# Optimization experiments

Hardware: AMD Instinct MI355X
Metric: run time of the kernel (lower is better)

## Reference

```python
import jax, jax.numpy as jnp
import numpy as np

B, S, H, L, NH, F, V, K, R = 64, 512, 256, 4, 8, 1024, 50265, 8, 25
DH = H // NH
EPS = 1e-5


def layernorm(x, g, b):
    mu = x.mean(-1, keepdims=True)
    var = ((x - mu) ** 2).mean(-1, keepdims=True)
    return (x - mu) * jax.lax.rsqrt(var + EPS) * g + b


def setup_inputs() -> dict:
    key = jax.random.key(0)
    ks = jax.random.split(key, 24)
    input_ids = jax.random.randint(ks[0], (B, S), 0, V, dtype=jnp.int64)
    # prefix attention mask with variable valid lengths (ragged sequences)
    lengths = jax.random.randint(ks[1], (B,), 16, S + 1)
    attention_mask = (jnp.arange(S)[None, :] < lengths[:, None]).astype(jnp.int32)
    sub_indices = jax.random.randint(ks[2], (B, K), 0, S, dtype=jnp.int64)
    obj_indices = jax.random.randint(ks[3], (B, K), 0, S, dtype=jnp.int64)
    sub_counts = jax.random.randint(ks[4], (B,), 0, K + 1, dtype=jnp.int32)
    obj_counts = jax.random.randint(ks[5], (B,), 0, K + 1, dtype=jnp.int32)
    sc = 0.02
    p = {
        'emb': jax.random.normal(ks[6], (V, H), jnp.float32) * sc,
        'Wqkv': jax.random.normal(ks[7], (L, H, 3 * H), jnp.float32) * sc,
        'bqkv': jnp.zeros((L, 3 * H), jnp.float32),
        'Wo': jax.random.normal(ks[8], (L, H, H), jnp.float32) * sc,
        'bo': jnp.zeros((L, H), jnp.float32),
        'ln1_g': jnp.ones((L, H), jnp.float32), 'ln1_b': jnp.zeros((L, H), jnp.float32),
        'ln2_g': jnp.ones((L, H), jnp.float32), 'ln2_b': jnp.zeros((L, H), jnp.float32),
        'W1': jax.random.normal(ks[9], (L, H, F), jnp.float32) * sc,
        'b1': jnp.zeros((L, F), jnp.float32),
        'W2': jax.random.normal(ks[10], (L, F, H), jnp.float32) * sc,
        'b2': jnp.zeros((L, H), jnp.float32),
        'lnf_g': jnp.ones((H,), jnp.float32), 'lnf_b': jnp.zeros((H,), jnp.float32),
        'mW1': jax.random.normal(ks[11], (3 * H, H), jnp.float32) * sc,
        'mb1': jnp.zeros((H,), jnp.float32),
        'mW2': jax.random.normal(ks[12], (H, R), jnp.float32) * sc,
        'mb2': jnp.zeros((R,), jnp.float32),
    }
    return dict(input_ids=input_ids, attention_mask=attention_mask,
                sub_indices=sub_indices, sub_counts=sub_counts,
                obj_indices=obj_indices, obj_counts=obj_counts, **p)


def _encoder(input_ids, attention_mask, emb, Wqkv, bqkv, Wo, bo,
             ln1_g, ln1_b, ln2_g, ln2_b, W1, b1, W2, b2, lnf_g, lnf_b):
    x = emb[input_ids]  # [B,S,H]
    kbias = jnp.where(attention_mask[:, None, None, :] > 0, 0.0, -1e9)  # mask keys
    scale = 1.0 / np.sqrt(DH)
    for l in range(L):  # small fixed layer loop
        qkv = x @ Wqkv[l] + bqkv[l]
        q, k, v = jnp.split(qkv, 3, axis=-1)
        q = q.reshape(B, S, NH, DH).transpose(0, 2, 1, 3)
        k = k.reshape(B, S, NH, DH).transpose(0, 2, 1, 3)
        v = v.reshape(B, S, NH, DH).transpose(0, 2, 1, 3)
        scores = jnp.einsum('bhqd,bhkd->bhqk', q, k) * scale + kbias
        attn = jax.nn.softmax(scores, axis=-1)
        o = jnp.einsum('bhqk,bhkd->bhqd', attn, v).transpose(0, 2, 1, 3).reshape(B, S, H)
        x = layernorm(x + o @ Wo[l] + bo[l], ln1_g[l], ln1_b[l])
        h = jax.nn.relu(x @ W1[l] + b1[l]) @ W2[l] + b2[l]
        x = layernorm(x + h, ln2_g[l], ln2_b[l])
    return layernorm(x, lnf_g, lnf_b)


def _pooled(seq, idx, counts):
    g = jnp.take_along_axis(seq, idx[:, :, None], axis=1)  # [B,K,H]
    m = (jnp.arange(K)[None, :] < counts[:, None]).astype(seq.dtype)
    s = (g * m[:, :, None]).sum(1)
    c = counts.astype(seq.dtype)[:, None]
    return jnp.where(c > 0, s / jnp.maximum(c, 1.0), 0.0)  # zeros if no indices


def reference(input_ids, attention_mask, sub_indices, sub_counts, obj_indices, obj_counts,
              emb, Wqkv, bqkv, Wo, bo, ln1_g, ln1_b, ln2_g, ln2_b,
              W1, b1, W2, b2, lnf_g, lnf_b, mW1, mb1, mW2, mb2):
    seq = _encoder(input_ids, attention_mask, emb, Wqkv, bqkv, Wo, bo,
                   ln1_g, ln1_b, ln2_g, ln2_b, W1, b1, W2, b2, lnf_g, lnf_b)
    sub = _pooled(seq, sub_indices, sub_counts)
    obj = _pooled(seq, obj_indices, obj_counts)
    mask = attention_mask.astype(seq.dtype)
    lens = mask.sum(1)[:, None]
    story = jnp.where(lens > 0, (seq * mask[:, :, None]).sum(1) / jnp.maximum(lens, 1.0),
                      seq.mean(1))
    feat = jnp.concatenate([sub, obj, story], axis=-1)  # [B,3H]
    logits = jax.nn.relu(feat @ mW1 + mb1) @ mW2 + mb2
    return logits
```

## Files before the change

kernel.cpp:

```cpp
#include <hip/hip_runtime.h>
#include <hip/hip_bf16.h>


typedef __hip_bfloat16 bf16;
typedef __attribute__((ext_vector_type(8))) short short8;
typedef __attribute__((ext_vector_type(4))) float f32x4;

#define S_LEN 512
#define H_DIM 256
#define NTOK  32768

__device__ __forceinline__ void gload_lds16(const void* g, void* l) {
  __builtin_amdgcn_global_load_lds(
      (const __attribute__((address_space(1))) unsigned int*)g,
      (__attribute__((address_space(3))) unsigned int*)l, 16, 0, 0);
}

__device__ __forceinline__ unsigned short f2bu(float x) {
  bf16 t = __float2bfloat16(x);
  return *reinterpret_cast<unsigned short*>(&t);
}

__global__ __launch_bounds__(64) void lens_kernel(
    const int* __restrict__ amask, int* __restrict__ ntiles,
    int* __restrict__ lenb) {
  const int b = blockIdx.x, t = threadIdx.x;
  int c = 0;
#pragma unroll
  for (int i = 0; i < 8; ++i) c += amask[b * S_LEN + t + i * 64];
#pragma unroll
  for (int off = 1; off < 64; off <<= 1) c += __shfl_xor(c, off);
  if (t == 0) {
    lenb[b] = c;
    ntiles[b] = (c + 63) >> 6;
  }
}

__global__ __launch_bounds__(256) void tcast_kernel(
    const float* __restrict__ in, bf16* __restrict__ out, int K, int N) {
  const int l = blockIdx.z;
  in  += (size_t)l * K * N;
  out += (size_t)l * K * N;
  __shared__ float t[32][33];
  const int n0 = blockIdx.x * 32, k0 = blockIdx.y * 32;
  const int c = threadIdx.x & 31, r = threadIdx.x >> 5;
#pragma unroll
  for (int rr = r; rr < 32; rr += 8)
    t[rr][c] = in[(size_t)(k0 + rr) * N + n0 + c];
  __syncthreads();
#pragma unroll
  for (int rr = r; rr < 32; rr += 8)
    out[(size_t)(n0 + rr) * K + k0 + c] = __float2bfloat16(t[c][rr]);
}

__global__ __launch_bounds__(256) void embed_kernel(
    const int* __restrict__ ids, const float* __restrict__ emb,
    float* __restrict__ X, bf16* __restrict__ Xb) {
  size_t i4 = (size_t)blockIdx.x * 256 + threadIdx.x;
  int tok = (int)(i4 >> 6);
  int d4  = (int)(i4 & 63);
  float4 v = *(const float4*)&emb[(size_t)ids[tok] * H_DIM + d4 * 4];
  *(float4*)&X[i4 * 4] = v;
  ushort4 pk;
  pk.x = f2bu(v.x); pk.y = f2bu(v.y); pk.z = f2bu(v.z); pk.w = f2bu(v.w);
  *(ushort4*)&Xb[i4 * 4] = pk;
}

template<int MODE, bool RELU>
__global__ __launch_bounds__(256) void hgemm_kernel(
    const bf16* __restrict__ A, const bf16* __restrict__ Bt,
    const float* __restrict__ bias, float* __restrict__ Cf,
    bf16* __restrict__ Cb, bf16* __restrict__ Vt,
    int M, int N, int K) {
  __shared__ __align__(16) bf16 As[2][4096];
  __shared__ __align__(16) bf16 Bs[2][4096];
  const int tid = threadIdx.x;
  const int wv = tid >> 6, ln = tid & 63;
  const int fr = ln & 15, g4 = ln >> 4;
  const int wr = wv >> 1, wc = wv & 1;
  const int m0 = blockIdx.y * 128, n0 = blockIdx.x * 128;
  const int lr = tid >> 2, lk = (tid & 3) * 8;

#define STAGE_G(buf, kk) do {                                                  \
    const int kof_ = (kk) * 32;                                                \
    gload_lds16(A  + (size_t)(m0 + lr) * K + kof_ + lk,                        \
                &As[(buf)][wv * 512]);                                         \
    gload_lds16(A  + (size_t)(m0 + 64 + lr) * K + kof_ + lk,                   \
                &As[(buf)][2048 + wv * 512]);                                  \
    gload_lds16(Bt + (size_t)(n0 + lr) * K + kof_ + lk,                        \
                &Bs[(buf)][wv * 512]);                                         \
    gload_lds16(Bt + (size_t)(n0 + 64 + lr) * K + kof_ + lk,                   \
                &Bs[(buf)][2048 + wv * 512]);                                  \
  } while (0)

  f32x4 acc[4][4];
#pragma unroll
  for (int i = 0; i < 4; ++i)
#pragma unroll
    for (int j = 0; j < 4; ++j)
      acc[i][j] = (f32x4){0.f, 0.f, 0.f, 0.f};

  const int NT = K >> 5;
  STAGE_G(0, 0);
  __syncthreads();
  int cur = 0;
  for (int kt = 0; kt < NT; ++kt) {
    if (kt + 1 < NT) STAGE_G(cur ^ 1, kt + 1);
    short8 af[4], bfv[4];
#pragma unroll
    for (int i = 0; i < 4; ++i)
      af[i] = *(const short8*)&As[cur][(wr * 64 + i * 16 + fr) * 32 + g4 * 8];
#pragma unroll
    for (int j = 0; j < 4; ++j)
      bfv[j] = *(const short8*)&Bs[cur][(wc * 64 + j * 16 + fr) * 32 + g4 * 8];
#pragma unroll
    for (int i = 0; i < 4; ++i)
#pragma unroll
      for (int j = 0; j < 4; ++j)
        acc[i][j] = __builtin_amdgcn_mfma_f32_16x16x32_bf16(
            af[i], bfv[j], acc[i][j], 0, 0, 0);
    __syncthreads();
    cur ^= 1;
  }
#undef STAGE_G

  const int crow = g4 * 4, ccol = fr;
#pragma unroll
  for (int j = 0; j < 4; ++j) {
    const int n = n0 + wc * 64 + j * 16 + ccol;
    const float bv = bias[n];
#pragma unroll
    for (int i = 0; i < 4; ++i) {
      const int mbase = m0 + wr * 64 + i * 16 + crow;
#pragma unroll
      for (int r = 0; r < 4; ++r) {
        float o = acc[i][j][r] + bv;
        if (RELU) o = fmaxf(o, 0.f);
        const int m = mbase + r;
        if (MODE == 1) {
          Cb[(size_t)m * N + n] = __float2bfloat16(o);
        } else {
          if (n < 512) {
            Cb[(size_t)m * 768 + n] = __float2bfloat16(o);
          } else {
            const int hd = n - 512, hh = hd >> 5, dd = hd & 31;
            const int bb = m >> 9, ss = m & 511;
            const int ssw = (ss & ~63) | ((ss & 63) ^ ((dd & 7) << 3));
            Vt[(((size_t)bb * 8 + hh) * 32 + dd) * 512 + ssw] =
                __float2bfloat16(o);
          }
        }
      }
    }
  }
}

__global__ __launch_bounds__(256) void hgemm_ln_kernel(
    const bf16* __restrict__ A, const bf16* __restrict__ Bt,
    const float* __restrict__ bias, float* __restrict__ X,
    bf16* __restrict__ Xb, const float* __restrict__ g,
    const float* __restrict__ bt, int K) {
  __shared__ __align__(16) bf16 As[2][2048];
  __shared__ __align__(16) bf16 Bs[2][8192];
  __shared__ float rsum[4][64];
  __shared__ float rsq[4][64];
  const int tid = threadIdx.x;
  const int wv = tid >> 6;
  const int ln = tid & 63;
  const int fr = ln & 15, g4 = ln >> 4;
  const int m0 = blockIdx.x * 64;

#define STAGE_L(buf, kk) do {                                                  \
    const int kof_ = (kk) * 32;                                                \
    gload_lds16(A + (size_t)(m0 + (tid >> 2)) * K + kof_ + (tid & 3) * 8,      \
                &As[(buf)][wv * 512]);                                         \
    _Pragma("unroll")                                                          \
    for (int e = 0; e < 4; ++e) {                                              \
      const int vt = e * 256 + tid;                                            \
      gload_lds16(Bt + (size_t)(vt >> 2) * K + kof_ + (vt & 3) * 8,            \
                  &Bs[(buf)][e * 2048 + wv * 512]);                            \
    }                                                                          \
  } while (0)

  f32x4 acc[4][4];
#pragma unroll
  for (int i = 0; i < 4; ++i)
#pragma unroll
    for (int j = 0; j < 4; ++j)
      acc[i][j] = (f32x4){0.f, 0.f, 0.f, 0.f};

  const int NT = K >> 5;
  STAGE_L(0, 0);
  __syncthreads();
  int cur = 0;
  for (int kt = 0; kt < NT; ++kt) {
    if (kt + 1 < NT) STAGE_L(cur ^ 1, kt + 1);
    short8 af[4], bfv[4];
#pragma unroll
    for (int i = 0; i < 4; ++i)
      af[i] = *(const short8*)&As[cur][(i * 16 + fr) * 32 + g4 * 8];
#pragma unroll
    for (int j = 0; j < 4; ++j)
      bfv[j] = *(const short8*)&Bs[cur][(wv * 64 + j * 16 + fr) * 32 + g4 * 8];
#pragma unroll
    for (int i = 0; i < 4; ++i)
#pragma unroll
      for (int j = 0; j < 4; ++j)
        acc[i][j] = __builtin_amdgcn_mfma_f32_16x16x32_bf16(
            af[i], bfv[j], acc[i][j], 0, 0, 0);
    __syncthreads();
    cur ^= 1;
  }
#undef STAGE_L

  float gj[4], bj[4], bsj[4];
#pragma unroll
  for (int j = 0; j < 4; ++j) {
    const int n = wv * 64 + j * 16 + fr;
    gj[j] = g[n]; bj[j] = bt[n]; bsj[j] = bias[n];
  }
#pragma unroll
  for (int i = 0; i < 4; ++i) {
#pragma unroll
    for (int r = 0; r < 4; ++r) {
      const int m = m0 + i * 16 + g4 * 4 + r;
#pragma unroll
      for (int j = 0; j < 4; ++j)
        acc[i][j][r] += bsj[j] + X[(size_t)m * 256 + wv * 64 + j * 16 + fr];
    }
  }
#pragma unroll
  for (int i = 0; i < 4; ++i) {
#pragma unroll
    for (int r = 0; r < 4; ++r) {
      float sp = acc[i][0][r] + acc[i][1][r] + acc[i][2][r] + acc[i][3][r];
      float qp = acc[i][0][r] * acc[i][0][r] + acc[i][1][r] * acc[i][1][r] +
                 acc[i][2][r] * acc[i][2][r] + acc[i][3][r] * acc[i][3][r];
#pragma unroll
      for (int off = 1; off < 16; off <<= 1) {
        sp += __shfl_xor(sp, off);
        qp += __shfl_xor(qp, off);
      }
      if (fr == 0) {
        const int ri = i * 16 + g4 * 4 + r;
        rsum[wv][ri] = sp;
        rsq[wv][ri] = qp;
      }
    }
  }
  __syncthreads();
#pragma unroll
  for (int i = 0; i < 4; ++i) {
#pragma unroll
    for (int r = 0; r < 4; ++r) {
      const int ri = i * 16 + g4 * 4 + r;
      const float tot = rsum[0][ri] + rsum[1][ri] + rsum[2][ri] + rsum[3][ri];
      const float tq = rsq[0][ri] + rsq[1][ri] + rsq[2][ri] + rsq[3][ri];
      const float mu = tot * (1.0f / 256.0f);
      const float var = tq * (1.0f / 256.0f) - mu * mu;
      const float rstd = rsqrtf(var + 1e-5f);
      const int m = m0 + ri;
#pragma unroll
      for (int j = 0; j < 4; ++j) {
        const float o = (acc[i][j][r] - mu) * rstd * gj[j] + bj[j];
        const size_t idx = (size_t)m * 256 + wv * 64 + j * 16 + fr;
        X[idx] = o;
        Xb[idx] = __float2bfloat16(o);
      }
    }
  }
}

__global__ __launch_bounds__(256) void attn_mfma_kernel(
    const bf16* __restrict__ QKVb, const bf16* __restrict__ Vt,
    const int* __restrict__ amask, const int* __restrict__ ntiles,
    bf16* __restrict__ Ob) {
  const int b = blockIdx.z, h = blockIdx.y, q0 = blockIdx.x * 64;
  const int tid = threadIdx.x;
  const int wv = tid >> 6, ln = tid & 63;
  const int fr = ln & 15, g4 = ln >> 4;
  const int f8 = (fr & 7) << 3;
  const int bh32 = (b * 8 + h) * 32;
  __shared__ __align__(16) bf16 Qs[2048];
  __shared__ __align__(16) bf16 Ks[2][2048];
  __shared__ __align__(16) bf16 Vs[2][2048];
  __shared__ __align__(16) bf16 Ps[4096];
  __shared__ __align__(16) float Ms[64];

  const int nt = ntiles[b];

#define STAGE_A(buf, kt_) do {                                                 \
    const int k0_ = (kt_) * 64;                                                \
    gload_lds16(QKVb + (size_t)(b * S_LEN + k0_ + (tid >> 2)) * 768 + 256 +    \
                    h * 32 + (tid & 3) * 8,                                    \
                &Ks[(buf)][wv * 512]);                                         \
    gload_lds16(Vt + (size_t)(bh32 + (tid >> 3)) * 512 + k0_ + (tid & 7) * 8,  \
                &Vs[(buf)][wv * 512]);                                         \
    if ((kt_) == nt - 1 && tid < 64)                                           \
      Ms[tid] = (amask[b * S_LEN + k0_ + tid] != 0) ? 0.f : -1e9f;             \
  } while (0)

  gload_lds16(QKVb + (size_t)(b * S_LEN + q0 + (tid >> 2)) * 768 + h * 32 +
                  (tid & 3) * 8,
              &Qs[wv * 512]);
  STAGE_A(0, 0);
  __syncthreads();
  const short8 qb = *(const short8*)&Qs[(wv * 16 + fr) * 32 + g4 * 8];

  f32x4 accO[2];
  accO[0] = (f32x4){0.f, 0.f, 0.f, 0.f};
  accO[1] = (f32x4){0.f, 0.f, 0.f, 0.f};
  float mrun = -1e30f, lrun = 0.f;
  const float SC2 = 0.17677669529663687f * 1.4426950408889634f;
  const int srcq = 20 * g4;

  int cur = 0;
  for (int kt = 0; kt < nt; ++kt) {
    if (kt + 1 < nt) STAGE_A(cur ^ 1, kt + 1);
    const bool bnd = (kt == nt - 1);

    f32x4 st[4];
#pragma unroll
    for (int kb = 0; kb < 4; ++kb) {
      const short8 kf = *(const short8*)&Ks[cur][(kb * 16 + fr) * 32 + g4 * 8];
      f32x4 z = (f32x4){0.f, 0.f, 0.f, 0.f};
      st[kb] = __builtin_amdgcn_mfma_f32_16x16x32_bf16(kf, qb, z, 0, 0, 0);
    }

    float p[16];
    float mx = -1e30f;
    if (bnd) {
#pragma unroll
      for (int kb = 0; kb < 4; ++kb) {
        const f32x4 mv = ((const f32x4*)Ms)[kb * 4 + g4];
#pragma unroll
        for (int rr = 0; rr < 4; ++rr) {
          const float v = st[kb][rr] * SC2 + mv[rr];
          p[kb * 4 + rr] = v;
          mx = fmaxf(mx, v);
        }
      }
    } else {
#pragma unroll
      for (int kb = 0; kb < 4; ++kb) {
#pragma unroll
        for (int rr = 0; rr < 4; ++rr) {
          const float v = st[kb][rr] * SC2;
          p[kb * 4 + rr] = v;
          mx = fmaxf(mx, v);
        }
      }
    }
    mx = fmaxf(mx, __shfl_xor(mx, 16));
    mx = fmaxf(mx, __shfl_xor(mx, 32));
    const float mnew = fmaxf(mrun, mx);
    const float corr = exp2f(mrun - mnew);
    float ps = 0.f;
#pragma unroll
    for (int i = 0; i < 16; ++i) {
      const float e = exp2f(p[i] - mnew);
      p[i] = e;
      ps += e;
    }
    ps += __shfl_xor(ps, 16);
    ps += __shfl_xor(ps, 32);
    lrun = lrun * corr + ps;
    mrun = mnew;

#pragma unroll
    for (int rr = 0; rr < 4; ++rr) {
      const float cs = __shfl(corr, srcq + rr);
      accO[0][rr] *= cs;
      accO[1][rr] *= cs;
    }

#pragma unroll
    for (int kb = 0; kb < 4; ++kb) {
      ushort4 w4;
      w4.x = f2bu(p[kb * 4 + 0]);
      w4.y = f2bu(p[kb * 4 + 1]);
      w4.z = f2bu(p[kb * 4 + 2]);
      w4.w = f2bu(p[kb * 4 + 3]);
      *(ushort4*)&Ps[wv * 1024 + fr * 64 + ((kb * 16 + g4 * 4) ^ f8)] = w4;
    }

#pragma unroll
    for (int kk = 0; kk < 2; ++kk) {
      const short8 pa = *(const short8*)
          &Ps[wv * 1024 + fr * 64 + ((kk * 32 + g4 * 8) ^ f8)];
#pragma unroll
      for (int df = 0; df < 2; ++df) {
        const short8 vb = *(const short8*)
            &Vs[cur][(df * 16 + fr) * 64 + ((kk * 32 + g4 * 8) ^ f8)];
        accO[df] = __builtin_amdgcn_mfma_f32_16x16x32_bf16(
            pa, vb, accO[df], 0, 0, 0);
      }
    }
    __syncthreads();
    cur ^= 1;
  }
#undef STAGE_A

  const float inv = 1.0f / lrun;
#pragma unroll
  for (int rr = 0; rr < 4; ++rr) {
    const float iv = __shfl(inv, srcq + rr);
    const int q = q0 + wv * 16 + g4 * 4 + rr;
    const size_t orow = ((size_t)b * S_LEN + q) * H_DIM + h * 32;
    Ob[orow + fr]      = __float2bfloat16(accO[0][rr] * iv);
    Ob[orow + 16 + fr] = __float2bfloat16(accO[1][rr] * iv);
  }
}

__global__ __launch_bounds__(256) void lnf_pool_kernel(
    float* __restrict__ X, const float* __restrict__ g,
    const float* __restrict__ bt, const int* __restrict__ amask,
    float* __restrict__ Pstory) {
  const int b = blockIdx.x, sg = blockIdx.y;
  const int tid = threadIdx.x, wv = tid >> 6, ln = tid & 63;
  const float4 gg = ((const float4*)g)[ln];
  const float4 bb = ((const float4*)bt)[ln];
  float ax = 0.f, ay = 0.f, az = 0.f, aw = 0.f;
  for (int t = wv; t < 64; t += 4) {
    const size_t tok = (size_t)b * S_LEN + sg * 64 + t;
    float4 v = ((const float4*)X)[tok * 64 + ln];
    float s = v.x + v.y + v.z + v.w;
#pragma unroll
    for (int off = 1; off < 64; off <<= 1) s += __shfl_xor(s, off);
    const float mu = s * (1.0f / 256.0f);
    const float dx = v.x - mu, dy = v.y - mu, dz = v.z - mu, dw = v.w - mu;
    float sq = dx * dx + dy * dy + dz * dz + dw * dw;
#pragma unroll
    for (int off = 1; off < 64; off <<= 1) sq += __shfl_xor(sq, off);
    const float rstd = rsqrtf(sq * (1.0f / 256.0f) + 1e-5f);
    float4 o;
    o.x = dx * rstd * gg.x + bb.x;
    o.y = dy * rstd * gg.y + bb.y;
    o.z = dz * rstd * gg.z + bb.z;
    o.w = dw * rstd * gg.w + bb.w;
    ((float4*)X)[tok * 64 + ln] = o;
    if (amask[tok]) { ax += o.x; ay += o.y; az += o.z; aw += o.w; }
  }
  __shared__ float part[4][256];
  part[wv][ln * 4 + 0] = ax;
  __syncthreads();
  part[wv][ln * 4 + 0] = ax;
  part[wv][ln * 4 + 1] = ay;
  part[wv][ln * 4 + 2] = az;
  part[wv][ln * 4 + 3] = aw;
  __syncthreads();
  const float tot = part[0][tid] + part[1][tid] + part[2][tid] + part[3][tid];
  Pstory[((size_t)b * 8 + sg) * 256 + tid] = tot;
}

__global__ __launch_bounds__(256) void poolc_kernel(
    const float* __restrict__ X, const float* __restrict__ Pstory,
    const int* __restrict__ lenb,
    const int* __restrict__ sub_idx, const int* __restrict__ sub_cnt,
    const int* __restrict__ obj_idx, const int* __restrict__ obj_cnt,
    float* __restrict__ feat) {
  const int b = blockIdx.x, c = threadIdx.x;
  float s = 0.f;
#pragma unroll
  for (int i = 0; i < 8; ++i) s += Pstory[((size_t)b * 8 + i) * 256 + c];
  feat[(size_t)b * 768 + 512 + c] = s / (float)lenb[b];
  const float* xb = X + (size_t)b * S_LEN * H_DIM;
  {
    const int cc = sub_cnt[b];
    float s2 = 0.f;
    for (int j = 0; j < cc; ++j)
      s2 += xb[(size_t)sub_idx[b * 8 + j] * H_DIM + c];
    feat[(size_t)b * 768 + c] = (cc > 0) ? s2 / (float)cc : 0.f;
  }
  {
    const int cc = obj_cnt[b];
    float s2 = 0.f;
    for (int j = 0; j < cc; ++j)
      s2 += xb[(size_t)obj_idx[b * 8 + j] * H_DIM + c];
    feat[(size_t)b * 768 + 256 + c] = (cc > 0) ? s2 / (float)cc : 0.f;
  }
}

__global__ __launch_bounds__(256) void cls_kernel(
    const float* __restrict__ feat, const float* __restrict__ mW1,
    const float* __restrict__ mb1, const float* __restrict__ mW2,
    const float* __restrict__ mb2, float* __restrict__ out) {
  const int b = blockIdx.x, t = threadIdx.x;
  __shared__ float fs[768];
  __shared__ float hid[256];
#pragma unroll
  for (int e = 0; e < 3; ++e) fs[t + e * 256] = feat[(size_t)b * 768 + t + e * 256];
  __syncthreads();
  float acc = mb1[t];
  for (int k = 0; k < 768; ++k) acc += fs[k] * mW1[(size_t)k * 256 + t];
  hid[t] = fmaxf(acc, 0.f);
  __syncthreads();
  if (t < 25) {
    float o = mb2[t];
    for (int j = 0; j < 256; ++j) o += hid[j] * mW2[j * 25 + t];
    out[b * 25 + t] = o;
  }
}

extern "C" void kernel_launch(void* const* d_in, const int* in_sizes, int n_in,
                              void* d_out, int out_size, void* d_ws, size_t ws_size,
                              hipStream_t stream) {
  const int*   input_ids = (const int*)d_in[0];
  const int*   amask     = (const int*)d_in[1];
  const int*   sub_idx   = (const int*)d_in[2];
  const int*   sub_cnt   = (const int*)d_in[3];
  const int*   obj_idx   = (const int*)d_in[4];
  const int*   obj_cnt   = (const int*)d_in[5];
  const float* emb  = (const float*)d_in[6];
  const float* Wqkv = (const float*)d_in[7];
  const float* bqkv = (const float*)d_in[8];
  const float* Wo   = (const float*)d_in[9];
  const float* bo   = (const float*)d_in[10];
  const float* ln1g = (const float*)d_in[11];
  const float* ln1b = (const float*)d_in[12];
  const float* ln2g = (const float*)d_in[13];
  const float* ln2b = (const float*)d_in[14];
  const float* W1   = (const float*)d_in[15];
  const float* b1   = (const float*)d_in[16];
  const float* W2   = (const float*)d_in[17];
  const float* b2   = (const float*)d_in[18];
  const float* lnfg = (const float*)d_in[19];
  const float* lnfb = (const float*)d_in[20];
  const float* mW1  = (const float*)d_in[21];
  const float* mb1  = (const float*)d_in[22];
  const float* mW2  = (const float*)d_in[23];
  const float* mb2  = (const float*)d_in[24];
  float* out = (float*)d_out;

  char* w = (char*)d_ws;
  float* X    = (float*)w;                         w += (size_t)NTOK * 256 * 4;
  bf16*  Xb   = (bf16*)w;                          w += (size_t)NTOK * 256 * 2;
  bf16*  QKVb = (bf16*)w;                          w += (size_t)NTOK * 768 * 2;
  bf16*  Vtg  = (bf16*)w;                          w += (size_t)NTOK * 256 * 2;
  bf16*  Ob   = (bf16*)w;                          w += (size_t)NTOK * 256 * 2;
  bf16*  Wqkvt= (bf16*)w;                          w += (size_t)4 * 768 * 256 * 2;
  bf16*  Wot  = (bf16*)w;                          w += (size_t)4 * 256 * 256 * 2;
  bf16*  W1t  = (bf16*)w;                          w += (size_t)4 * 1024 * 256 * 2;
  bf16*  W2t  = (bf16*)w;                          w += (size_t)4 * 256 * 1024 * 2;
  float* feat = (float*)w;                         w += (size_t)64 * 768 * 4;
  float* Pstory = (float*)w;                       w += (size_t)64 * 8 * 256 * 4;
  int*   ntiles = (int*)w;                         w += 256;
  int*   lenb   = (int*)w;                         w += 256;
  bf16*  Hb   = QKVb;

  lens_kernel<<<64, 64, 0, stream>>>(amask, ntiles, lenb);
  tcast_kernel<<<dim3(24, 8, 4), 256, 0, stream>>>(Wqkv, Wqkvt, 256, 768);
  tcast_kernel<<<dim3(8, 8, 4), 256, 0, stream>>>(Wo, Wot, 256, 256);
  tcast_kernel<<<dim3(32, 8, 4), 256, 0, stream>>>(W1, W1t, 256, 1024);
  tcast_kernel<<<dim3(8, 32, 4), 256, 0, stream>>>(W2, W2t, 1024, 256);

  embed_kernel<<<8192, 256, 0, stream>>>(input_ids, emb, X, Xb);

  for (int l = 0; l < 4; ++l) {
    const bf16* Wqkvt_l = Wqkvt + (size_t)l * 768 * 256;
    const bf16* Wot_l   = Wot + (size_t)l * 256 * 256;
    const bf16* W1t_l   = W1t + (size_t)l * 1024 * 256;
    const bf16* W2t_l   = W2t + (size_t)l * 256 * 1024;

    hgemm_kernel<2, false><<<dim3(6, 256), 256, 0, stream>>>(
        Xb, Wqkvt_l, bqkv + (size_t)l * 768, nullptr, QKVb, Vtg, NTOK, 768, 256);
    attn_mfma_kernel<<<dim3(8, 8, 64), 256, 0, stream>>>(
        QKVb, Vtg, amask, ntiles, Ob);
    hgemm_ln_kernel<<<512, 256, 0, stream>>>(
        Ob, Wot_l, bo + (size_t)l * 256, X, Xb,
        ln1g + l * 256, ln1b + l * 256, 256);
    hgemm_kernel<1, true><<<dim3(8, 256), 256, 0, stream>>>(
        Xb, W1t_l, b1 + (size_t)l * 1024, nullptr, Hb, nullptr, NTOK, 1024, 256);
    hgemm_ln_kernel<<<512, 256, 0, stream>>>(
        Hb, W2t_l, b2 + (size_t)l * 256, X, Xb,
        ln2g + l * 256, ln2b + l * 256, 1024);
  }
  lnf_pool_kernel<<<dim3(64, 8), 256, 0, stream>>>(X, lnfg, lnfb, amask, Pstory);
  poolc_kernel<<<64, 256, 0, stream>>>(X, Pstory, lenb, sub_idx, sub_cnt,
                                       obj_idx, obj_cnt, feat);
  cls_kernel<<<64, 256, 0, stream>>>(feat, mW1, mb1, mW2, mb2, out);
}
```

Baseline: 828.4 us.

## Sort attention batches by length, prescale Q, lazy softmax rescale, fuse pooling

Adds a kernel that ranks batches by tile count so the attention grid dispatches the longest sequences first, which should reduce tail imbalance from ragged lengths. Folds the softmax scale and log2e into Q when the QKV GEMM writes its output, removing a multiply per score. Rescales the output accumulator only when the running max grows by more than a threshold, and uses tree reductions for max and sum. Q staging reuses the P buffer to cut LDS use, which adds an extra barrier. The pooling and classifier kernels are fused, and a duplicated LDS store with its barrier is removed.

```diff
diff --git a/kernel.cpp b/kernel.cpp
--- a/kernel.cpp
+++ b/kernel.cpp
@@ -9,6 +9,7 @@
 #define S_LEN 512
 #define H_DIM 256
 #define NTOK  32768
+#define QSCALE 0.25503488f
 
 __device__ __forceinline__ void gload_lds16(const void* g, void* l) {
   __builtin_amdgcn_global_load_lds(
@@ -34,6 +35,18 @@
     lenb[b] = c;
     ntiles[b] = (c + 63) >> 6;
   }
+}
+
+__global__ __launch_bounds__(64) void order_kernel(
+    const int* __restrict__ ntiles, int* __restrict__ ordb) {
+  const int b = threadIdx.x;
+  const int ntb = ntiles[b];
+  int rank = 0;
+  for (int j = 0; j < 64; ++j) {
+    const int ntj = __shfl(ntb, j);
+    rank += (ntj > ntb) || (ntj == ntb && j < b);
+  }
+  ordb[rank] = b;
 }
 
 __global__ __launch_bounds__(256) void tcast_kernel(
@@ -141,7 +154,8 @@
           Cb[(size_t)m * N + n] = __float2bfloat16(o);
         } else {
           if (n < 512) {
-            Cb[(size_t)m * 768 + n] = __float2bfloat16(o);
+            const float oo = (n < 256) ? o * QSCALE : o;
+            Cb[(size_t)m * 768 + n] = __float2bfloat16(oo);
           } else {
             const int hd = n - 512, hh = hd >> 5, dd = hd & 31;
             const int bb = m >> 9, ss = m & 511;
@@ -274,14 +288,14 @@
 __global__ __launch_bounds__(256) void attn_mfma_kernel(
     const bf16* __restrict__ QKVb, const bf16* __restrict__ Vt,
     const int* __restrict__ amask, const int* __restrict__ ntiles,
-    bf16* __restrict__ Ob) {
-  const int b = blockIdx.z, h = blockIdx.y, q0 = blockIdx.x * 64;
+    const int* __restrict__ ordb, bf16* __restrict__ Ob) {
+  const int b = ordb[blockIdx.z];
+  const int h = blockIdx.y, q0 = blockIdx.x * 64;
   const int tid = threadIdx.x;
   const int wv = tid >> 6, ln = tid & 63;
   const int fr = ln & 15, g4 = ln >> 4;
   const int f8 = (fr & 7) << 3;
   const int bh32 = (b * 8 + h) * 32;
-  __shared__ __align__(16) bf16 Qs[2048];
   __shared__ __align__(16) bf16 Ks[2][2048];
   __shared__ __align__(16) bf16 Vs[2][2048];
   __shared__ __align__(16) bf16 Ps[4096];
@@ -302,16 +316,16 @@
 
   gload_lds16(QKVb + (size_t)(b * S_LEN + q0 + (tid >> 2)) * 768 + h * 32 +
                   (tid & 3) * 8,
-              &Qs[wv * 512]);
+              &Ps[wv * 512]);
   STAGE_A(0, 0);
   __syncthreads();
-  const short8 qb = *(const short8*)&Qs[(wv * 16 + fr) * 32 + g4 * 8];
+  const short8 qb = *(const short8*)&Ps[(wv * 16 + fr) * 32 + g4 * 8];
+  __syncthreads();
 
   f32x4 accO[2];
   accO[0] = (f32x4){0.f, 0.f, 0.f, 0.f};
   accO[1] = (f32x4){0.f, 0.f, 0.f, 0.f};
   float mrun = -1e30f, lrun = 0.f;
-  const float SC2 = 0.17677669529663687f * 1.4426950408889634f;
   const int srcq = 20 * g4;
 
   int cur = 0;
@@ -328,51 +342,51 @@
     }
 
     float p[16];
-    float mx = -1e30f;
     if (bnd) {
 #pragma unroll
       for (int kb = 0; kb < 4; ++kb) {
         const f32x4 mv = ((const f32x4*)Ms)[kb * 4 + g4];
 #pragma unroll
-        for (int rr = 0; rr < 4; ++rr) {
-          const float v = st[kb][rr] * SC2 + mv[rr];
-          p[kb * 4 + rr] = v;
-          mx = fmaxf(mx, v);
-        }
+        for (int rr = 0; rr < 4; ++rr) p[kb * 4 + rr] = st[kb][rr] + mv[rr];
       }
     } else {
 #pragma unroll
-      for (int kb = 0; kb < 4; ++kb) {
-#pragma unroll
-        for (int rr = 0; rr < 4; ++rr) {
-          const float v = st[kb][rr] * SC2;
-          p[kb * 4 + rr] = v;
-          mx = fmaxf(mx, v);
-        }
-      }
-    }
+      for (int kb = 0; kb < 4; ++kb)
+#pragma unroll
+        for (int rr = 0; rr < 4; ++rr) p[kb * 4 + rr] = st[kb][rr];
+    }
+
+    const float a0 = fmaxf(fmaxf(p[0], p[1]), p[2]);
+    const float a1 = fmaxf(fmaxf(p[3], p[4]), p[5]);
+    const float a2 = fmaxf(fmaxf(p[6], p[7]), p[8]);
+    const float a3 = fmaxf(fmaxf(p[9], p[10]), p[11]);
+    const float a4 = fmaxf(fmaxf(p[12], p[13]), p[14]);
+    float mx = fmaxf(fmaxf(fmaxf(a0, a1), fmaxf(a2, a3)), fmaxf(a4, p[15]));
     mx = fmaxf(mx, __shfl_xor(mx, 16));
     mx = fmaxf(mx, __shfl_xor(mx, 32));
-    const float mnew = fmaxf(mrun, mx);
-    const float corr = exp2f(mrun - mnew);
-    float ps = 0.f;
-#pragma unroll
-    for (int i = 0; i < 16; ++i) {
-      const float e = exp2f(p[i] - mnew);
-      p[i] = e;
-      ps += e;
-    }
+
+    float corr = 1.f;
+    if (!__all(mx <= mrun + 8.f)) {
+      const float mnew = fmaxf(mrun, mx);
+      corr = exp2f(mrun - mnew);
+      mrun = mnew;
+#pragma unroll
+      for (int rr = 0; rr < 4; ++rr) {
+        const float cs = __shfl(corr, srcq + rr);
+        accO[0][rr] *= cs;
+        accO[1][rr] *= cs;
+      }
+    }
+
+#pragma unroll
+    for (int i = 0; i < 16; ++i) p[i] = exp2f(p[i] - mrun);
+    const float b0 = p[0] + p[1], b1 = p[2] + p[3], b2 = p[4] + p[5],
+                b3 = p[6] + p[7], b4 = p[8] + p[9], b5 = p[10] + p[11],
+                b6 = p[12] + p[13], b7 = p[14] + p[15];
+    float ps = ((b0 + b1) + (b2 + b3)) + ((b4 + b5) + (b6 + b7));
     ps += __shfl_xor(ps, 16);
     ps += __shfl_xor(ps, 32);
     lrun = lrun * corr + ps;
-    mrun = mnew;
-
-#pragma unroll
-    for (int rr = 0; rr < 4; ++rr) {
-      const float cs = __shfl(corr, srcq + rr);
-      accO[0][rr] *= cs;
-      accO[1][rr] *= cs;
-    }
 
 #pragma unroll
     for (int kb = 0; kb < 4; ++kb) {
@@ -443,8 +457,6 @@
   }
   __shared__ float part[4][256];
   part[wv][ln * 4 + 0] = ax;
-  __syncthreads();
-  part[wv][ln * 4 + 0] = ax;
   part[wv][ln * 4 + 1] = ay;
   part[wv][ln * 4 + 2] = az;
   part[wv][ln * 4 + 3] = aw;
@@ -453,43 +465,38 @@
   Pstory[((size_t)b * 8 + sg) * 256 + tid] = tot;
 }
 
-__global__ __launch_bounds__(256) void poolc_kernel(
+__global__ __launch_bounds__(256) void poolcls_kernel(
     const float* __restrict__ X, const float* __restrict__ Pstory,
     const int* __restrict__ lenb,
     const int* __restrict__ sub_idx, const int* __restrict__ sub_cnt,
     const int* __restrict__ obj_idx, const int* __restrict__ obj_cnt,
-    float* __restrict__ feat) {
-  const int b = blockIdx.x, c = threadIdx.x;
-  float s = 0.f;
-#pragma unroll
-  for (int i = 0; i < 8; ++i) s += Pstory[((size_t)b * 8 + i) * 256 + c];
-  feat[(size_t)b * 768 + 512 + c] = s / (float)lenb[b];
+    const float* __restrict__ mW1, const float* __restrict__ mb1,
+    const float* __restrict__ mW2, const float* __restrict__ mb2,
+    float* __restrict__ out) {
+  const int b = blockIdx.x, t = threadIdx.x;
+  __shared__ float fs[768];
+  __shared__ float hid[256];
   const float* xb = X + (size_t)b * S_LEN * H_DIM;
+  {
+    float s = 0.f;
+#pragma unroll
+    for (int i = 0; i < 8; ++i) s += Pstory[((size_t)b * 8 + i) * 256 + t];
+    fs[512 + t] = s / (float)lenb[b];
+  }
   {
     const int cc = sub_cnt[b];
     float s2 = 0.f;
     for (int j = 0; j < cc; ++j)
-      s2 += xb[(size_t)sub_idx[b * 8 + j] * H_DIM + c];
-    feat[(size_t)b * 768 + c] = (cc > 0) ? s2 / (float)cc : 0.f;
+      s2 += xb[(size_t)sub_idx[b * 8 + j] * H_DIM + t];
+    fs[t] = (cc > 0) ? s2 / (float)cc : 0.f;
   }
   {
     const int cc = obj_cnt[b];
     float s2 = 0.f;
     for (int j = 0; j < cc; ++j)
-      s2 += xb[(size_t)obj_idx[b * 8 + j] * H_DIM + c];
-    feat[(size_t)b * 768 + 256 + c] = (cc > 0) ? s2 / (float)cc : 0.f;
-  }
-}
-
-__global__ __launch_bounds__(256) void cls_kernel(
-    const float* __restrict__ feat, const float* __restrict__ mW1,
-    const float* __restrict__ mb1, const float* __restrict__ mW2,
-    const float* __restrict__ mb2, float* __restrict__ out) {
-  const int b = blockIdx.x, t = threadIdx.x;
-  __shared__ float fs[768];
-  __shared__ float hid[256];
-#pragma unroll
-  for (int e = 0; e < 3; ++e) fs[t + e * 256] = feat[(size_t)b * 768 + t + e * 256];
+      s2 += xb[(size_t)obj_idx[b * 8 + j] * H_DIM + t];
+    fs[256 + t] = (cc > 0) ? s2 / (float)cc : 0.f;
+  }
   __syncthreads();
   float acc = mb1[t];
   for (int k = 0; k < 768; ++k) acc += fs[k] * mW1[(size_t)k * 256 + t];
@@ -542,13 +549,14 @@
   bf16*  Wot  = (bf16*)w;                          w += (size_t)4 * 256 * 256 * 2;
   bf16*  W1t  = (bf16*)w;                          w += (size_t)4 * 1024 * 256 * 2;
   bf16*  W2t  = (bf16*)w;                          w += (size_t)4 * 256 * 1024 * 2;
-  float* feat = (float*)w;                         w += (size_t)64 * 768 * 4;
   float* Pstory = (float*)w;                       w += (size_t)64 * 8 * 256 * 4;
   int*   ntiles = (int*)w;                         w += 256;
   int*   lenb   = (int*)w;                         w += 256;
+  int*   ordb   = (int*)w;                         w += 256;
   bf16*  Hb   = QKVb;
 
   lens_kernel<<<64, 64, 0, stream>>>(amask, ntiles, lenb);
+  order_kernel<<<1, 64, 0, stream>>>(ntiles, ordb);
   tcast_kernel<<<dim3(24, 8, 4), 256, 0, stream>>>(Wqkv, Wqkvt, 256, 768);
   tcast_kernel<<<dim3(8, 8, 4), 256, 0, stream>>>(Wo, Wot, 256, 256);
   tcast_kernel<<<dim3(32, 8, 4), 256, 0, stream>>>(W1, W1t, 256, 1024);
@@ -565,7 +573,7 @@
     hgemm_kernel<2, false><<<dim3(6, 256), 256, 0, stream>>>(
         Xb, Wqkvt_l, bqkv + (size_t)l * 768, nullptr, QKVb, Vtg, NTOK, 768, 256);
     attn_mfma_kernel<<<dim3(8, 8, 64), 256, 0, stream>>>(
-        QKVb, Vtg, amask, ntiles, Ob);
+        QKVb, Vtg, amask, ntiles, ordb, Ob);
     hgemm_ln_kernel<<<512, 256, 0, stream>>>(
         Ob, Wot_l, bo + (size_t)l * 256, X, Xb,
         ln1g + l * 256, ln1b + l * 256, 256);
@@ -576,7 +584,7 @@
         ln2g + l * 256, ln2b + l * 256, 1024);
   }
   lnf_pool_kernel<<<dim3(64, 8), 256, 0, stream>>>(X, lnfg, lnfb, amask, Pstory);
-  poolc_kernel<<<64, 256, 0, stream>>>(X, Pstory, lenb, sub_idx, sub_cnt,
-                                       obj_idx, obj_cnt, feat);
-  cls_kernel<<<64, 256, 0, stream>>>(feat, mW1, mb1, mW2, mb2, out);
-}
+  poolcls_kernel<<<64, 256, 0, stream>>>(X, Pstory, lenb, sub_idx, sub_cnt,
+                                         obj_idx, obj_cnt, mW1, mb1, mW2, mb2,
+                                         out);
+}
```

Result: faster. 809.0 us (-2.3%).
